# Optimization experiments

Hardware: AMD Instinct MI355X
Metric: run time of the kernel (lower is better)

Reference implementation:

```python
import jax, jax.numpy as jnp
import numpy as np

B, S, UNITS = 32, 2048, 512

def setup_inputs() -> dict:
    key = jax.random.key(0)
    ks = jax.random.split(key, 8)
    sc = 1.0 / np.sqrt(UNITS)
    return {
        "s_prev": jax.random.normal(ks[0], (B, UNITS), jnp.float32),
        "hidden_states": jax.random.normal(ks[1], (B, S, UNITS), jnp.float32),
        "W_kernel": jax.random.normal(ks[2], (UNITS, UNITS), jnp.float32) * sc,
        "W_bias": jnp.zeros((UNITS,), jnp.float32),
        "U_kernel": jax.random.normal(ks[3], (UNITS, UNITS), jnp.float32) * sc,
        "U_bias": jnp.zeros((UNITS,), jnp.float32),
        "V_kernel": jax.random.normal(ks[4], (UNITS, 1), jnp.float32) * sc,
        "V_bias": jnp.zeros((1,), jnp.float32),
    }

def reference(s_prev, hidden_states, W_kernel, W_bias, U_kernel, U_bias, V_kernel, V_bias):
    # NOTE: faithful to the source code: U is applied to s_prev, W to hidden_states,
    # and the context is computed as softmax-weights * s_prev (as written, a quirk
    # of the original module), summed over the sequence axis.
    first = s_prev @ U_kernel + U_bias                      # (B, units)
    second = hidden_states @ W_kernel + W_bias              # (B, S, units)
    score = jnp.tanh(first[:, None, :] + second) @ V_kernel + V_bias  # (B, S, 1)
    weights = jax.nn.softmax(score, axis=1)                 # (B, S, 1)
    context = jnp.sum(weights * s_prev[:, None, :], axis=1) # (B, units)
    return context, weights
```

## Files before the change

### kernel.cpp

```cpp
#include <hip/hip_runtime.h>

#define NBATCH 32
#define SEQ    2048
#define NU     512
#define ASTR   36

typedef __attribute__((ext_vector_type(8)))  short bf16x8;
typedef __attribute__((ext_vector_type(16))) float f32x16;

__device__ __forceinline__ short bf16_rne(float f) {
  union { float f; unsigned u; } v; v.f = f;
  unsigned r = v.u + 0x7fffu + ((v.u >> 16) & 1u);
  return (short)(r >> 16);
}

__device__ __forceinline__ unsigned pk2(float lo, float hi) {
  return __builtin_amdgcn_perm(__float_as_uint(hi), __float_as_uint(lo), 0x07060302u);
}

__device__ __forceinline__ float fast_tanh(float x) {
  float ax = __builtin_fabsf(x);
  float t  = __expf(-2.0f * ax);
  float r  = (1.0f - t) / (1.0f + t);
  return x < 0.0f ? -r : r;
}

__global__ __launch_bounds__(256) void prep_all(const float* __restrict__ W,
                                                const float* __restrict__ sp,
                                                const float* __restrict__ U,
                                                const float* __restrict__ Ub,
                                                const float* __restrict__ Wb,
                                                short* __restrict__ Wt,
                                                float* __restrict__ first) {
  __shared__ float srow[NU];
  if (blockIdx.x < 1024) {
    int idx = blockIdx.x * 256 + threadIdx.x;
    int u = idx >> 9, k = idx & 511;
    Wt[(size_t)u * NU + k] = bf16_rne(W[(size_t)k * NU + u]);
  } else {
    int blk = blockIdx.x - 1024;
    int b = blk >> 1, half = blk & 1, t = threadIdx.x;
    srow[t]       = sp[b * NU + t];
    srow[t + 256] = sp[b * NU + t + 256];
    __syncthreads();
    int col = half * 256 + t;
    float acc = Ub[col] + Wb[col];
    #pragma unroll 8
    for (int k = 0; k < NU; ++k) acc += srow[k] * U[(size_t)k * NU + col];
    first[b * NU + col] = acc;
  }
}

__global__ __launch_bounds__(256, 3) void attn_main(
    const float* __restrict__ h,
    const short* __restrict__ Wt,
    const float* __restrict__ first,
    const float* __restrict__ V,
    float* __restrict__ s0)
{
  __shared__ short Alds[2][128 * ASTR];
  __shared__ short Blds[2][128 * ASTR];
  __shared__ float scores_lds[128];

  const int tid  = threadIdx.x;
  const int lane = tid & 63;
  const int w    = tid >> 6;
  const int wr   = w >> 1, wc = w & 1;
  const int l31  = lane & 31, hi = lane >> 5;

  const int bid = blockIdx.x;
  const int lb  = (bid & 7) * 256 + (bid >> 3);
  const int panel = lb >> 2, q = lb & 3;
  const int rowbase = panel * 128;
  const int b = panel >> 4;

  const int arow  = tid >> 1;
  const int ahalf = tid & 1;
  const float* hA = h + (size_t)(rowbase + arow) * NU + ahalf * 16;
  const int awr   = arow * ASTR + ahalf * 16;
  const short* bsrc = Wt + (size_t)(q * 128 + arow) * NU + ahalf * 16;

  const int rA0 = (wr * 64 +  0 + l31) * ASTR + hi * 8;
  const int rA1 = (wr * 64 + 32 + l31) * ASTR + hi * 8;
  const int rB0 = (wc * 64 +  0 + l31) * ASTR + hi * 8;
  const int rB1 = (wc * 64 + 32 + l31) * ASTR + hi * 8;

  f32x16 acc[2][2];
  #pragma unroll
  for (int rt = 0; rt < 2; ++rt)
    #pragma unroll
    for (int ct = 0; ct < 2; ++ct)
      #pragma unroll
      for (int r = 0; r < 16; ++r) acc[rt][ct][r] = 0.f;

  float4 ha0, ha1, ha2, ha3;
  float4 hb0, hb1, hb2, hb3;
  int4   bq0, bq1;

  #define CVT_WRITE(dst, H0, H1, H2, H3)                                   \
    {                                                                      \
      uint4 u0, u1;                                                        \
      u0.x = pk2(H0.x, H0.y); u0.y = pk2(H0.z, H0.w);                      \
      u0.z = pk2(H1.x, H1.y); u0.w = pk2(H1.z, H1.w);                      \
      u1.x = pk2(H2.x, H2.y); u1.y = pk2(H2.z, H2.w);                      \
      u1.z = pk2(H3.x, H3.y); u1.w = pk2(H3.z, H3.w);                      \
      *reinterpret_cast<uint4*>(&Alds[dst][awr])     = u0;                 \
      *reinterpret_cast<uint4*>(&Alds[dst][awr + 8]) = u1;                 \
      *reinterpret_cast<int4*>(&Blds[dst][awr])      = bq0;                \
      *reinterpret_cast<int4*>(&Blds[dst][awr + 8])  = bq1;                \
    }

  #define COMPUTE(cur)                                                     \
    _Pragma("unroll")                                                      \
    for (int ks = 0; ks < 2; ++ks) {                                       \
      bf16x8 af0, af1, bf0, bf1;                                           \
      af0 = *reinterpret_cast<const bf16x8*>(&Alds[cur][rA0 + ks * 16]);   \
      af1 = *reinterpret_cast<const bf16x8*>(&Alds[cur][rA1 + ks * 16]);   \
      bf0 = *reinterpret_cast<const bf16x8*>(&Blds[cur][rB0 + ks * 16]);   \
      bf1 = *reinterpret_cast<const bf16x8*>(&Blds[cur][rB1 + ks * 16]);   \
      acc[0][0] = __builtin_amdgcn_mfma_f32_32x32x16_bf16(af0, bf0, acc[0][0], 0, 0, 0); \
      acc[0][1] = __builtin_amdgcn_mfma_f32_32x32x16_bf16(af0, bf1, acc[0][1], 0, 0, 0); \
      acc[1][0] = __builtin_amdgcn_mfma_f32_32x32x16_bf16(af1, bf0, acc[1][0], 0, 0, 0); \
      acc[1][1] = __builtin_amdgcn_mfma_f32_32x32x16_bf16(af1, bf1, acc[1][1], 0, 0, 0); \
    }

  bq0 = *reinterpret_cast<const int4*>(bsrc);
  bq1 = *reinterpret_cast<const int4*>(bsrc + 8);
  ha0 = *reinterpret_cast<const float4*>(hA + 0);
  ha1 = *reinterpret_cast<const float4*>(hA + 4);
  ha2 = *reinterpret_cast<const float4*>(hA + 8);
  ha3 = *reinterpret_cast<const float4*>(hA + 12);
  CVT_WRITE(0, ha0, ha1, ha2, ha3);
  hb0 = *reinterpret_cast<const float4*>(hA + 32);
  hb1 = *reinterpret_cast<const float4*>(hA + 36);
  hb2 = *reinterpret_cast<const float4*>(hA + 40);
  hb3 = *reinterpret_cast<const float4*>(hA + 44);
  __syncthreads();

  for (int kt2 = 0; kt2 < 7; ++kt2) {
    const int kt = kt2 * 2;
    bq0 = *reinterpret_cast<const int4*>(bsrc + (kt + 1) * 32);
    bq1 = *reinterpret_cast<const int4*>(bsrc + (kt + 1) * 32 + 8);
    {
      const float* p = hA + (kt + 2) * 32;
      ha0 = *reinterpret_cast<const float4*>(p + 0);
      ha1 = *reinterpret_cast<const float4*>(p + 4);
      ha2 = *reinterpret_cast<const float4*>(p + 8);
      ha3 = *reinterpret_cast<const float4*>(p + 12);
    }
    COMPUTE(0);
    CVT_WRITE(1, hb0, hb1, hb2, hb3);
    __syncthreads();

    bq0 = *reinterpret_cast<const int4*>(bsrc + (kt + 2) * 32);
    bq1 = *reinterpret_cast<const int4*>(bsrc + (kt + 2) * 32 + 8);
    {
      const float* p = hA + (kt + 3) * 32;
      hb0 = *reinterpret_cast<const float4*>(p + 0);
      hb1 = *reinterpret_cast<const float4*>(p + 4);
      hb2 = *reinterpret_cast<const float4*>(p + 8);
      hb3 = *reinterpret_cast<const float4*>(p + 12);
    }
    COMPUTE(1);
    CVT_WRITE(0, ha0, ha1, ha2, ha3);
    __syncthreads();
  }

  bq0 = *reinterpret_cast<const int4*>(bsrc + 15 * 32);
  bq1 = *reinterpret_cast<const int4*>(bsrc + 15 * 32 + 8);
  COMPUTE(0);
  CVT_WRITE(1, hb0, hb1, hb2, hb3);
  __syncthreads();

  COMPUTE(1);

  #undef CVT_WRITE
  #undef COMPUTE

  float fv[2], vv[2];
  #pragma unroll
  for (int ct = 0; ct < 2; ++ct) {
    int col = q * 128 + wc * 64 + ct * 32 + l31;
    fv[ct] = first[b * NU + col];
    vv[ct] = V[col];
  }
  float part[2][16];
  #pragma unroll
  for (int rt = 0; rt < 2; ++rt) {
    #pragma unroll
    for (int r = 0; r < 16; ++r) {
      float p = 0.f;
      #pragma unroll
      for (int ct = 0; ct < 2; ++ct)
        p += vv[ct] * fast_tanh(fv[ct] + acc[rt][ct][r]);
      #pragma unroll
      for (int m = 1; m < 32; m <<= 1) p += __shfl_xor(p, m, 64);
      part[rt][r] = p;
    }
  }
  __syncthreads();
  if (wc == 0 && l31 == 0) {
    #pragma unroll
    for (int rt = 0; rt < 2; ++rt)
      #pragma unroll
      for (int r = 0; r < 16; ++r)
        scores_lds[wr * 64 + rt * 32 + (r & 3) + 8 * (r >> 2) + 4 * hi] = part[rt][r];
  }
  __syncthreads();
  if (wc == 1 && l31 == 0) {
    #pragma unroll
    for (int rt = 0; rt < 2; ++rt)
      #pragma unroll
      for (int r = 0; r < 16; ++r)
        scores_lds[wr * 64 + rt * 32 + (r & 3) + 8 * (r >> 2) + 4 * hi] += part[rt][r];
  }
  __syncthreads();
  if (tid < 128) atomicAdd(&s0[rowbase + tid], scores_lds[tid]);
}

__global__ __launch_bounds__(256) void softmax_ctx(const float* __restrict__ sp,
                                                   float* __restrict__ out) {
  const int b = blockIdx.x;
  const int t = threadIdx.x;
  float* wgt = out + NBATCH * NU + (size_t)b * SEQ;
  __shared__ float red[4];

  float v[8];
  float mx = -1e30f;
  #pragma unroll
  for (int i = 0; i < 8; ++i) { v[i] = wgt[t + i * 256]; mx = fmaxf(mx, v[i]); }
  #pragma unroll
  for (int m = 1; m < 64; m <<= 1) mx = fmaxf(mx, __shfl_xor(mx, m, 64));
  if ((t & 63) == 0) red[t >> 6] = mx;
  __syncthreads();
  mx = fmaxf(fmaxf(red[0], red[1]), fmaxf(red[2], red[3]));
  __syncthreads();

  float se = 0.f;
  #pragma unroll
  for (int i = 0; i < 8; ++i) { v[i] = __expf(v[i] - mx); se += v[i]; }
  #pragma unroll
  for (int m = 1; m < 64; m <<= 1) se += __shfl_xor(se, m, 64);
  if ((t & 63) == 0) red[t >> 6] = se;
  __syncthreads();
  se = red[0] + red[1] + red[2] + red[3];
  __syncthreads();

  const float inv = 1.0f / se;
  float sw = 0.f;
  #pragma unroll
  for (int i = 0; i < 8; ++i) { float wi = v[i] * inv; wgt[t + i * 256] = wi; sw += wi; }
  #pragma unroll
  for (int m = 1; m < 64; m <<= 1) sw += __shfl_xor(sw, m, 64);
  if ((t & 63) == 0) red[t >> 6] = sw;
  __syncthreads();
  sw = red[0] + red[1] + red[2] + red[3];

  out[b * NU + t]       = sp[b * NU + t] * sw;
  out[b * NU + t + 256] = sp[b * NU + t + 256] * sw;
}

extern "C" void kernel_launch(void* const* d_in, const int* in_sizes, int n_in,
                              void* d_out, int out_size, void* d_ws, size_t ws_size,
                              hipStream_t stream) {
  (void)in_sizes; (void)n_in; (void)out_size; (void)ws_size;
  const float* s_prev = (const float*)d_in[0];
  const float* h      = (const float*)d_in[1];
  const float* Wk     = (const float*)d_in[2];
  const float* Wb     = (const float*)d_in[3];
  const float* Uk     = (const float*)d_in[4];
  const float* Ub     = (const float*)d_in[5];
  const float* Vk     = (const float*)d_in[6];

  float* out   = (float*)d_out;
  float* first = (float*)d_ws;
  short* Wt    = (short*)((char*)d_ws + 65536);
  float* s0    = out + NBATCH * NU;

  hipMemsetAsync(s0, 0, (size_t)NBATCH * SEQ * sizeof(float), stream);
  prep_all   <<<1088, 256, 0, stream>>>(Wk, s_prev, Uk, Ub, Wb, Wt, first);
  attn_main  <<<2048, 256, 0, stream>>>(h, Wt, first, Vk, s0);
  softmax_ctx<<<  32, 256, 0, stream>>>(s_prev, out);
}
```

Measured before the change: 113.5 us.

## Load W tiles straight into LDS with global_load_lds and XOR swizzle

The B operand (transposed bf16 W) now goes from global memory directly into LDS with the async global_load_lds intrinsic instead of through registers. To keep the MFMA fragment reads free of bank conflicts without padding, prep_all stores W with an XOR swizzle on k chunks, and the compute reads undo it. Plain syncthreads are replaced by explicit vmcnt/lgkmcnt waits plus s_barrier so outstanding h loads stay in flight. This saves VGPRs and VALU store work but depends on getting the manual waitcnt accounting right.

```diff
diff --git a/kernel.cpp b/kernel.cpp
--- a/kernel.cpp
+++ b/kernel.cpp
@@ -30,13 +30,14 @@
                                                 const float* __restrict__ U,
                                                 const float* __restrict__ Ub,
                                                 const float* __restrict__ Wb,
-                                                short* __restrict__ Wt,
+                                                short* __restrict__ WtSw,
                                                 float* __restrict__ first) {
   __shared__ float srow[NU];
   if (blockIdx.x < 1024) {
     int idx = blockIdx.x * 256 + threadIdx.x;
-    int u = idx >> 9, k = idx & 511;
-    Wt[(size_t)u * NU + k] = bf16_rne(W[(size_t)k * NU + u]);
+    int col = idx >> 9, k = idx & 511;
+    int ksrc = k ^ ((col & 3) << 3);
+    WtSw[idx] = bf16_rne(W[(size_t)ksrc * NU + col]);
   } else {
     int blk = blockIdx.x - 1024;
     int b = blk >> 1, half = blk & 1, t = threadIdx.x;
@@ -53,13 +54,13 @@
 
 __global__ __launch_bounds__(256, 3) void attn_main(
     const float* __restrict__ h,
-    const short* __restrict__ Wt,
+    const short* __restrict__ WtSw,
     const float* __restrict__ first,
     const float* __restrict__ V,
     float* __restrict__ s0)
 {
   __shared__ short Alds[2][128 * ASTR];
-  __shared__ short Blds[2][128 * ASTR];
+  __shared__ short Blds[2][128 * 32];
   __shared__ float scores_lds[128];
 
   const int tid  = threadIdx.x;
@@ -78,12 +79,25 @@
   const int ahalf = tid & 1;
   const float* hA = h + (size_t)(rowbase + arow) * NU + ahalf * 16;
   const int awr   = arow * ASTR + ahalf * 16;
-  const short* bsrc = Wt + (size_t)(q * 128 + arow) * NU + ahalf * 16;
-
-  const int rA0 = (wr * 64 +  0 + l31) * ASTR + hi * 8;
-  const int rA1 = (wr * 64 + 32 + l31) * ASTR + hi * 8;
-  const int rB0 = (wc * 64 +  0 + l31) * ASTR + hi * 8;
-  const int rB1 = (wc * 64 + 32 + l31) * ASTR + hi * 8;
+
+  const short* bsrcB = WtSw + (size_t)(q * 128 + w * 16 + (lane >> 2)) * NU + (lane & 3) * 8;
+
+  #define GLOAD_B(buf, ktn)                                                              \
+    {                                                                                    \
+      __builtin_amdgcn_global_load_lds(                                                  \
+          (const __attribute__((address_space(1))) unsigned*)(bsrcB + (ktn) * 32),       \
+          (__attribute__((address_space(3))) unsigned*)(&Blds[buf][w * 512]), 16, 0, 0); \
+      __builtin_amdgcn_global_load_lds(                                                  \
+          (const __attribute__((address_space(1))) unsigned*)(bsrcB + (ktn) * 32 + 64 * NU), \
+          (__attribute__((address_space(3))) unsigned*)(&Blds[buf][2048 + w * 512]), 16, 0, 0); \
+      asm volatile("" ::: "memory");                                                     \
+    }
+
+  const int rA0 = (wr * 64 + l31) * ASTR + hi * 8;
+  const int rA1 = rA0 + 32 * ASTR;
+  const int colb0 = wc * 64 + l31;
+  const int swb   = colb0 & 3;
+  const int bB0 = colb0 * 32, bB1 = bB0 + 32 * 32;
 
   f32x16 acc[2][2];
   #pragma unroll
@@ -95,87 +109,92 @@
 
   float4 ha0, ha1, ha2, ha3;
   float4 hb0, hb1, hb2, hb3;
-  int4   bq0, bq1;
-
-  #define CVT_WRITE(dst, H0, H1, H2, H3)                                   \
-    {                                                                      \
-      uint4 u0, u1;                                                        \
-      u0.x = pk2(H0.x, H0.y); u0.y = pk2(H0.z, H0.w);                      \
-      u0.z = pk2(H1.x, H1.y); u0.w = pk2(H1.z, H1.w);                      \
-      u1.x = pk2(H2.x, H2.y); u1.y = pk2(H2.z, H2.w);                      \
-      u1.z = pk2(H3.x, H3.y); u1.w = pk2(H3.z, H3.w);                      \
-      *reinterpret_cast<uint4*>(&Alds[dst][awr])     = u0;                 \
-      *reinterpret_cast<uint4*>(&Alds[dst][awr + 8]) = u1;                 \
-      *reinterpret_cast<int4*>(&Blds[dst][awr])      = bq0;                \
-      *reinterpret_cast<int4*>(&Blds[dst][awr + 8])  = bq1;                \
-    }
-
-  #define COMPUTE(cur)                                                     \
-    _Pragma("unroll")                                                      \
-    for (int ks = 0; ks < 2; ++ks) {                                       \
-      bf16x8 af0, af1, bf0, bf1;                                           \
-      af0 = *reinterpret_cast<const bf16x8*>(&Alds[cur][rA0 + ks * 16]);   \
-      af1 = *reinterpret_cast<const bf16x8*>(&Alds[cur][rA1 + ks * 16]);   \
-      bf0 = *reinterpret_cast<const bf16x8*>(&Blds[cur][rB0 + ks * 16]);   \
-      bf1 = *reinterpret_cast<const bf16x8*>(&Blds[cur][rB1 + ks * 16]);   \
+
+  #define LOAD_H(V0, V1, V2, V3, ktn)                                       \
+    {                                                                       \
+      const float* p = hA + (ktn) * 32;                                     \
+      V0 = *reinterpret_cast<const float4*>(p + 0);                         \
+      V1 = *reinterpret_cast<const float4*>(p + 4);                         \
+      V2 = *reinterpret_cast<const float4*>(p + 8);                         \
+      V3 = *reinterpret_cast<const float4*>(p + 12);                        \
+    }
+
+  #define CVT_WRITE(dst, V0, V1, V2, V3)                                    \
+    {                                                                       \
+      uint4 u0, u1;                                                         \
+      u0.x = pk2(V0.x, V0.y); u0.y = pk2(V0.z, V0.w);                       \
+      u0.z = pk2(V1.x, V1.y); u0.w = pk2(V1.z, V1.w);                       \
+      u1.x = pk2(V2.x, V2.y); u1.y = pk2(V2.z, V2.w);                       \
+      u1.z = pk2(V3.x, V3.y); u1.w = pk2(V3.z, V3.w);                       \
+      *reinterpret_cast<uint4*>(&Alds[dst][awr])     = u0;                  \
+      *reinterpret_cast<uint4*>(&Alds[dst][awr + 8]) = u1;                  \
+    }
+
+  #define COMPUTE(cur)                                                      \
+    _Pragma("unroll")                                                       \
+    for (int ks = 0; ks < 2; ++ks) {                                        \
+      const int sb = ((ks * 2 + hi) ^ swb) << 3;                            \
+      bf16x8 af0, af1, bf0, bf1;                                            \
+      af0 = *reinterpret_cast<const bf16x8*>(&Alds[cur][rA0 + ks * 16]);    \
+      af1 = *reinterpret_cast<const bf16x8*>(&Alds[cur][rA1 + ks * 16]);    \
+      bf0 = *reinterpret_cast<const bf16x8*>(&Blds[cur][bB0 + sb]);         \
+      bf1 = *reinterpret_cast<const bf16x8*>(&Blds[cur][bB1 + sb]);         \
       acc[0][0] = __builtin_amdgcn_mfma_f32_32x32x16_bf16(af0, bf0, acc[0][0], 0, 0, 0); \
       acc[0][1] = __builtin_amdgcn_mfma_f32_32x32x16_bf16(af0, bf1, acc[0][1], 0, 0, 0); \
       acc[1][0] = __builtin_amdgcn_mfma_f32_32x32x16_bf16(af1, bf0, acc[1][0], 0, 0, 0); \
       acc[1][1] = __builtin_amdgcn_mfma_f32_32x32x16_bf16(af1, bf1, acc[1][1], 0, 0, 0); \
     }
 
-  bq0 = *reinterpret_cast<const int4*>(bsrc);
-  bq1 = *reinterpret_cast<const int4*>(bsrc + 8);
-  ha0 = *reinterpret_cast<const float4*>(hA + 0);
-  ha1 = *reinterpret_cast<const float4*>(hA + 4);
-  ha2 = *reinterpret_cast<const float4*>(hA + 8);
-  ha3 = *reinterpret_cast<const float4*>(hA + 12);
+  #define BAR_CNT(N)                                                        \
+    asm volatile("s_waitcnt vmcnt(" #N ") lgkmcnt(0)" ::: "memory");        \
+    __builtin_amdgcn_s_barrier();                                           \
+    asm volatile("" ::: "memory");
+
+  GLOAD_B(0, 0);
+  LOAD_H(ha0, ha1, ha2, ha3, 0);
   CVT_WRITE(0, ha0, ha1, ha2, ha3);
-  hb0 = *reinterpret_cast<const float4*>(hA + 32);
-  hb1 = *reinterpret_cast<const float4*>(hA + 36);
-  hb2 = *reinterpret_cast<const float4*>(hA + 40);
-  hb3 = *reinterpret_cast<const float4*>(hA + 44);
-  __syncthreads();
-
-  for (int kt2 = 0; kt2 < 7; ++kt2) {
+  LOAD_H(hb0, hb1, hb2, hb3, 1);
+  BAR_CNT(4);
+
+  #pragma unroll 1
+  for (int kt2 = 0; kt2 < 6; ++kt2) {
     const int kt = kt2 * 2;
-    bq0 = *reinterpret_cast<const int4*>(bsrc + (kt + 1) * 32);
-    bq1 = *reinterpret_cast<const int4*>(bsrc + (kt + 1) * 32 + 8);
-    {
-      const float* p = hA + (kt + 2) * 32;
-      ha0 = *reinterpret_cast<const float4*>(p + 0);
-      ha1 = *reinterpret_cast<const float4*>(p + 4);
-      ha2 = *reinterpret_cast<const float4*>(p + 8);
-      ha3 = *reinterpret_cast<const float4*>(p + 12);
-    }
+    GLOAD_B(1, kt + 1);
+    LOAD_H(ha0, ha1, ha2, ha3, kt + 2);
     COMPUTE(0);
     CVT_WRITE(1, hb0, hb1, hb2, hb3);
-    __syncthreads();
-
-    bq0 = *reinterpret_cast<const int4*>(bsrc + (kt + 2) * 32);
-    bq1 = *reinterpret_cast<const int4*>(bsrc + (kt + 2) * 32 + 8);
-    {
-      const float* p = hA + (kt + 3) * 32;
-      hb0 = *reinterpret_cast<const float4*>(p + 0);
-      hb1 = *reinterpret_cast<const float4*>(p + 4);
-      hb2 = *reinterpret_cast<const float4*>(p + 8);
-      hb3 = *reinterpret_cast<const float4*>(p + 12);
-    }
+    BAR_CNT(4);
+    GLOAD_B(0, kt + 2);
+    LOAD_H(hb0, hb1, hb2, hb3, kt + 3);
     COMPUTE(1);
     CVT_WRITE(0, ha0, ha1, ha2, ha3);
-    __syncthreads();
-  }
-
-  bq0 = *reinterpret_cast<const int4*>(bsrc + 15 * 32);
-  bq1 = *reinterpret_cast<const int4*>(bsrc + 15 * 32 + 8);
+    BAR_CNT(4);
+  }
+
+  GLOAD_B(1, 13);
+  LOAD_H(ha0, ha1, ha2, ha3, 14);
   COMPUTE(0);
   CVT_WRITE(1, hb0, hb1, hb2, hb3);
-  __syncthreads();
-
+  BAR_CNT(4);
+
+  GLOAD_B(0, 14);
+  LOAD_H(hb0, hb1, hb2, hb3, 15);
   COMPUTE(1);
-
+  CVT_WRITE(0, ha0, ha1, ha2, ha3);
+  BAR_CNT(4);
+
+  GLOAD_B(1, 15);
+  COMPUTE(0);
+  CVT_WRITE(1, hb0, hb1, hb2, hb3);
+  BAR_CNT(0);
+
+  COMPUTE(1);
+
+  #undef GLOAD_B
+  #undef LOAD_H
   #undef CVT_WRITE
   #undef COMPUTE
+  #undef BAR_CNT
 
   float fv[2], vv[2];
   #pragma unroll
@@ -274,11 +293,11 @@
 
   float* out   = (float*)d_out;
   float* first = (float*)d_ws;
-  short* Wt    = (short*)((char*)d_ws + 65536);
+  short* WtSw  = (short*)((char*)d_ws + 65536);
   float* s0    = out + NBATCH * NU;
 
   hipMemsetAsync(s0, 0, (size_t)NBATCH * SEQ * sizeof(float), stream);
-  prep_all   <<<1088, 256, 0, stream>>>(Wk, s_prev, Uk, Ub, Wb, Wt, first);
-  attn_main  <<<2048, 256, 0, stream>>>(h, Wt, first, Vk, s0);
+  prep_all   <<<1088, 256, 0, stream>>>(Wk, s_prev, Uk, Ub, Wb, WtSw, first);
+  attn_main  <<<2048, 256, 0, stream>>>(h, WtSw, first, Vk, s0);
   softmax_ctx<<<  32, 256, 0, stream>>>(s_prev, out);
 }
```

After: 117.4 us. 3.4% more time.
